# Kernel tuning notes

Hardware: AMD Instinct MI355X
Metric: run time of the kernel (lower is better)

The kernel has to match this reference:

```python
import jax, jax.numpy as jnp
import numpy as np

EPS = 1e-12  # torch F.normalize eps


def _l2norm(x, axis):
    return x / jnp.maximum(jnp.linalg.norm(x, axis=axis, keepdims=True), EPS)


def setup_inputs() -> dict:
    key = jax.random.key(0)
    ks = jax.random.split(key, 8)
    B, N, D_in, H, K, D_out = 16, 1024, 1024, 512, 64, 1024
    return {
        "input_data": jax.random.normal(ks[0], (B, N, D_in), dtype=jnp.float32),
        "fc1_w": jax.random.normal(ks[1], (H, D_in), dtype=jnp.float32) * 0.02,
        "fc1_b": jax.random.normal(ks[2], (H,), dtype=jnp.float32) * 0.02,
        "conv_w": jax.random.normal(ks[3], (K, H), dtype=jnp.float32) * 0.1,
        "conv_b": jax.random.normal(ks[4], (K,), dtype=jnp.float32) * 0.1,
        "centroids": jax.random.normal(ks[5], (K, H), dtype=jnp.float32),
        "fc2_w": jax.random.normal(ks[6], (D_out, K * H), dtype=jnp.float32) * 0.01,
        "fc2_b": jax.random.normal(ks[7], (D_out,), dtype=jnp.float32) * 0.01,
    }


def reference(input_data, fc1_w, fc1_b, conv_w, conv_b, centroids, fc2_w, fc2_b):
    # fc1 + relu: [B, N, H]
    h = jax.nn.relu(jnp.einsum('bnd,hd->bnh', input_data, fc1_w) + fc1_b)
    # NetVLAD input layout: [B, H, N] (the (N,1) spatial dims collapse to N)
    x = jnp.swapaxes(h, 1, 2)
    # normalize descriptors across feature dim (F.normalize(x, p=2, dim=1))
    xn = _l2norm(x, axis=1)
    # 1x1-conv soft assignment -> softmax over clusters: [B, K, N]
    logits = jnp.einsum('kh,bhn->bkn', conv_w, xn) + conv_b[None, :, None]
    a = jax.nn.softmax(logits, axis=1)
    # vlad_{bkh} = sum_n a_{bkn} (xn_{bhn} - c_{kh})  (fused, no [B,K,H,N] tensor)
    vlad = jnp.einsum('bkn,bhn->bkh', a, xn) - a.sum(axis=-1)[:, :, None] * centroids[None]
    vlad = _l2norm(vlad, axis=2)              # intra-normalization
    vlad = vlad.reshape(vlad.shape[0], -1)    # [B, K*H]
    vlad = _l2norm(vlad, axis=1)              # global L2 norm
    # fc2 + relu: [B, out_dim]
    return jax.nn.relu(vlad @ fc2_w.T + fc2_b)
```

## Files before the change

kernel.cpp:

```cpp
#include <hip/hip_runtime.h>
#include <hip/hip_bf16.h>

typedef __bf16  bf16x8 __attribute__((ext_vector_type(8)));
typedef float   f32x4  __attribute__((ext_vector_type(4)));

#define DEV __device__ __forceinline__

DEV ushort f2b(float f){
  union { float f; unsigned u; } c; c.f = f;
  unsigned u = c.u;
  unsigned r = (u + 0x7FFFu + ((u >> 16) & 1u)) >> 16;
  return (ushort)r;
}
DEV float b2f(ushort h){
  union { unsigned u; float f; } c; c.u = ((unsigned)h) << 16;
  return c.f;
}
DEV float wredsum(float v){
  #pragma unroll
  for(int o = 32; o > 0; o >>= 1) v += __shfl_xor(v, o, 64);
  return v;
}
DEV float wredmax(float v){
  #pragma unroll
  for(int o = 32; o > 0; o >>= 1) v = fmaxf(v, __shfl_xor(v, o, 64));
  return v;
}
DEV void gload_lds16(const void* g, void* l){
  __builtin_amdgcn_global_load_lds(
      (const __attribute__((address_space(1))) void*)g,
      (__attribute__((address_space(3))) void*)l,
      16, 0, 0);
}
DEV bf16x8 cvt8(float4 a0, float4 a1){
  bf16x8 t;
  t[0]=(__bf16)a0.x; t[1]=(__bf16)a0.y; t[2]=(__bf16)a0.z; t[3]=(__bf16)a0.w;
  t[4]=(__bf16)a1.x; t[5]=(__bf16)a1.y; t[6]=(__bf16)a1.z; t[7]=(__bf16)a1.w;
  return t;
}

__global__ void prep(const float* __restrict__ W1, const float* __restrict__ CW,
                     const float* __restrict__ CB,
                     ushort* __restrict__ W1b, ushort* __restrict__ CWb,
                     float* __restrict__ CBp){
  int bid = blockIdx.x, tid = threadIdx.x;
  if(bid < 512){
    int i = bid * 256 + tid;
    float4 f = ((const float4*)W1)[i];
    ushort4 o; o.x = f2b(f.x); o.y = f2b(f.y); o.z = f2b(f.z); o.w = f2b(f.w);
    ((ushort4*)W1b)[i] = o;
  } else if(bid < 640){
    int i = (bid - 512) * 256 + tid;
    int k = i >> 9, h = i & 511;
    int seg = h >> 3, pos = h & 7;
    CWb[(k << 9) + ((seg ^ (k & 7)) << 3) + pos] = f2b(CW[i]);
  } else {
    if(tid < 128) CBp[tid] = (tid < 64) ? CB[tid] : 0.0f;
  }
}

__global__ __launch_bounds__(512) void fc1sm(
    const float* __restrict__ A, const ushort* __restrict__ B,
    const float* __restrict__ bias, const ushort* __restrict__ CWb,
    const float* __restrict__ CBp, ushort* __restrict__ XNT,
    ushort* __restrict__ AThi, ushort* __restrict__ ATlo)
{
  const int K = 1024;
  __shared__ __align__(16) char smem[149504];
  __shared__ float ssq_p[4][64];
  __shared__ float scale_s[64];
  const int tid = threadIdx.x, lane = tid & 63, wid = tid >> 6;
  const int bm0 = blockIdx.x * 64;
  const int wr = (wid >> 2) * 32;
  const int wc = (wid & 3) * 128;
  const int wcol = wid & 3;

  const int srow = tid >> 3;
  const int sseg = tid & 7;
  const char* asrc = (const char*)A + (size_t)(bm0 + srow) * 4096
                     + (sseg ^ (srow & 7)) * 16;
  const int bslot = (tid & 3) ^ ((tid >> 3) & 3);
  const ushort* bg = B + (size_t)(tid >> 2) * K + bslot * 8;

  f32x4 acc[2][8];
  #pragma unroll
  for(int i = 0; i < 2; i++)
    #pragma unroll
    for(int j = 0; j < 8; j++) acc[i][j] = (f32x4){0.f, 0.f, 0.f, 0.f};

  const int arow = lane & 15;
  const int khalf = lane >> 4;

#define STAGE_F1N(buf, kb) do { \
    gload_lds16(asrc + (kb), smem + (buf) * 8192 + tid * 16); \
    const ushort* bs_ = bg + ((kb) >> 2); \
    char* bd_ = smem + 16384 + (buf) * 32768 + tid * 16; \
    gload_lds16(bs_,           bd_); \
    gload_lds16(bs_ + 128 * K, bd_ + 8192); \
    gload_lds16(bs_ + 256 * K, bd_ + 16384); \
    gload_lds16(bs_ + 384 * K, bd_ + 24576); \
  } while(0)

  STAGE_F1N(0, 0);
  __syncthreads();

  int cur = 0;
  for(int ks = 0; ks < 32; ++ks){
    if(ks + 1 < 32) STAGE_F1N(cur ^ 1, (ks + 1) * 128);
    bf16x8 af[2], bfr[8];
    #pragma unroll
    for(int mi = 0; mi < 2; mi++){
      int r = wr + mi * 16 + arow;
      const char* base = smem + cur * 8192 + r * 128;
      float4 a0 = *(const float4*)(base + (((khalf * 2)     ^ (r & 7)) * 16));
      float4 a1 = *(const float4*)(base + (((khalf * 2 + 1) ^ (r & 7)) * 16));
      af[mi] = cvt8(a0, a1);
    }
    #pragma unroll
    for(int ni = 0; ni < 8; ni++){
      int r = wc + ni * 16 + arow;
      bfr[ni] = *(const bf16x8*)(smem + 16384 + cur * 32768
                                 + r * 64 + ((khalf ^ ((r >> 1) & 3)) * 16));
    }
    #pragma unroll
    for(int mi = 0; mi < 2; mi++)
      #pragma unroll
      for(int ni = 0; ni < 8; ni++)
        acc[mi][ni] = __builtin_amdgcn_mfma_f32_16x16x32_bf16(af[mi], bfr[ni], acc[mi][ni], 0, 0, 0);
    __syncthreads();
    cur ^= 1;
  }
#undef STAGE_F1N

  float bv[8];
  #pragma unroll
  for(int ni = 0; ni < 8; ni++) bv[ni] = bias[wc + ni * 16 + (lane & 15)];
  float p[2][4];
  #pragma unroll
  for(int mi = 0; mi < 2; mi++)
    #pragma unroll
    for(int i = 0; i < 4; i++){
      float s = 0.f;
      #pragma unroll
      for(int ni = 0; ni < 8; ni++){
        float v = fmaxf(acc[mi][ni][i] + bv[ni], 0.f);
        acc[mi][ni][i] = v;
        s += v * v;
      }
      p[mi][i] = s;
    }
  #pragma unroll
  for(int o = 1; o < 16; o <<= 1)
    #pragma unroll
    for(int mi = 0; mi < 2; mi++)
      #pragma unroll
      for(int i = 0; i < 4; i++)
        p[mi][i] += __shfl_xor(p[mi][i], o, 64);
  if((lane & 15) == 0){
    int g = lane >> 4;
    #pragma unroll
    for(int mi = 0; mi < 2; mi++)
      #pragma unroll
      for(int i = 0; i < 4; i++)
        ssq_p[wcol][wr + mi * 16 + g * 4 + i] = p[mi][i];
  }
  __syncthreads();
  if(tid < 64){
    float s = ssq_p[0][tid] + ssq_p[1][tid] + ssq_p[2][tid] + ssq_p[3][tid];
    scale_s[tid] = 1.0f / fmaxf(sqrtf(s), 1e-12f);
  }
  __syncthreads();

  ushort* Tb  = (ushort*)(smem + 81920);
  ushort* xnm = (ushort*)smem;
  #pragma unroll
  for(int mi = 0; mi < 2; mi++)
    #pragma unroll
    for(int i = 0; i < 4; i++){
      int rt = wr + mi * 16 + (lane >> 4) * 4 + i;
      float sc = scale_s[rt];
      #pragma unroll
      for(int ni = 0; ni < 8; ni++){
        int h = wc + ni * 16 + (lane & 15);
        ushort v = f2b(acc[mi][ni][i] * sc);
        Tb[h * 66 + rt] = v;
        xnm[rt * 520 + h] = v;
      }
    }
  __syncthreads();

  const int bb = bm0 >> 10, n0b = bm0 & 1023;
  {
    const char* tb = (const char*)smem + 81920 + tid * 132;
    unsigned tmp[32];
    #pragma unroll
    for(int j = 0; j < 32; j++) tmp[j] = *(const unsigned*)(tb + j * 4);
    ushort* dst = XNT + ((size_t)bb * 512 + tid) * 1024 + n0b;
    #pragma unroll
    for(int u = 0; u < 8; u++){
      uint4 w; w.x = tmp[u*4]; w.y = tmp[u*4+1]; w.z = tmp[u*4+2]; w.w = tmp[u*4+3];
      *(uint4*)(dst + u * 8) = w;
    }
  }
  __syncthreads();

  char* CWs = smem + 66560;
  #pragma unroll
  for(int pp = 0; pp < 8; pp++)
    gload_lds16((const char*)CWb + pp * 8192 + tid * 16, CWs + pp * 8192 + tid * 16);
  __syncthreads();

  float* as_ = (float*)(smem + 132096);
  const int nt = (wid >> 2) * 32, kt = (wid & 3) * 16;
  f32x4 acc2[2];
  acc2[0] = (f32x4){0.f,0.f,0.f,0.f};
  acc2[1] = (f32x4){0.f,0.f,0.f,0.f};
  const int kr = kt + arow;
  #pragma unroll
  for(int s = 0; s < 16; ++s){
    bf16x8 a0 = *(const bf16x8*)(smem + (size_t)(nt + arow) * 1040 + s * 64 + khalf * 16);
    bf16x8 a1 = *(const bf16x8*)(smem + (size_t)(nt + 16 + arow) * 1040 + s * 64 + khalf * 16);
    bf16x8 bw = *(const bf16x8*)(CWs + kr * 1024 + (((s * 4 + khalf) ^ (kr & 7)) * 16));
    acc2[0] = __builtin_amdgcn_mfma_f32_16x16x32_bf16(a0, bw, acc2[0], 0, 0, 0);
    acc2[1] = __builtin_amdgcn_mfma_f32_16x16x32_bf16(a1, bw, acc2[1], 0, 0, 0);
  }
  {
    float bv2 = CBp[kt + (lane & 15)];
    #pragma unroll
    for(int mi = 0; mi < 2; mi++)
      #pragma unroll
      for(int i = 0; i < 4; i++)
        as_[(nt + mi * 16 + (lane >> 4) * 4 + i) * 65 + kt + (lane & 15)] = acc2[mi][i] + bv2;
  }
  __syncthreads();

  #pragma unroll
  for(int i = 0; i < 8; i++){
    int rl = wid * 8 + i;
    float l = as_[rl * 65 + lane];
    float m = wredmax(l);
    float e = __expf(l - m);
    float s = wredsum(e);
    as_[rl * 65 + lane] = e / s;
  }
  __syncthreads();

  {
    const int nl = tid & 63, kq = tid >> 6;
    #pragma unroll
    for(int q = 0; q < 8; q++){
      int k = kq * 8 + q;
      float a = as_[nl * 65 + k];
      ushort hi = f2b(a);
      float lo = a - b2f(hi);
      size_t idx = ((size_t)bb * 64 + k) * 1024 + n0b + nl;
      AThi[idx] = hi;
      ATlo[idx] = f2b(lo);
    }
  }
}

__global__ __launch_bounds__(512) void vlad_mfma(
    const ushort* __restrict__ AThi, const ushort* __restrict__ ATlo,
    const ushort* __restrict__ XNT, const float* __restrict__ cent,
    ushort* __restrict__ vlb, float* __restrict__ ssq)
{
  __shared__ __align__(16) ushort Ah[2][16 * 32];
  __shared__ __align__(16) ushort Al[2][16 * 32];
  __shared__ __align__(16) ushort Xs[2][512 * 32];
  __shared__ float red[8][16];
  __shared__ float scale_s[16], ssqn_s[16];
  const int tid = threadIdx.x, lane = tid & 63, wid = tid >> 6;
  const int b = blockIdx.x, kg = blockIdx.y;
  const int k0 = kg * 16;
  const int hw = wid;
  const int arow = lane & 15, khalf = lane >> 4;

  const int xslot = (tid & 3) ^ ((tid >> 3) & 3);
  const ushort* xg = XNT + ((size_t)b * 512 + (tid >> 2)) * 1024 + xslot * 8;
  const int aslot = (lane & 3) ^ ((lane >> 3) & 3);
  const ushort* ahg = AThi + ((size_t)b * 64 + k0 + (lane >> 2)) * 1024 + aslot * 8;
  const ushort* alg = ATlo + ((size_t)b * 64 + k0 + (lane >> 2)) * 1024 + aslot * 8;

  f32x4 acc[4];
  #pragma unroll
  for(int i = 0; i < 4; i++) acc[i] = (f32x4){0.f, 0.f, 0.f, 0.f};
  f32x4 asum = (f32x4){0.f, 0.f, 0.f, 0.f};
  bf16x8 ones;
  #pragma unroll
  for(int j = 0; j < 8; j++) ones[j] = (__bf16)1.0f;

#define STAGE_VL(buf, n0v) do { \
    char* xd = (char*)&Xs[buf][0] + tid * 16; \
    gload_lds16(xg + (n0v),                xd); \
    gload_lds16(xg + (n0v) + 128 * 1024,   xd + 8192); \
    gload_lds16(xg + (n0v) + 256 * 1024,   xd + 16384); \
    gload_lds16(xg + (n0v) + 384 * 1024,   xd + 24576); \
    if(wid == 0)      gload_lds16(ahg + (n0v), (char*)&Ah[buf][0] + lane * 16); \
    else if(wid == 1) gload_lds16(alg + (n0v), (char*)&Al[buf][0] + lane * 16); \
  } while(0)

  STAGE_VL(0, 0);
  __syncthreads();

  int cur = 0;
  for(int ks = 0; ks < 32; ++ks){
    if(ks + 1 < 32) STAGE_VL(cur ^ 1, (ks + 1) * 32);
    bf16x8 ah, al, bfr[4];
    {
      int sl = khalf ^ ((arow >> 1) & 3);
      ah = *(const bf16x8*)&Ah[cur][arow * 32 + sl * 8];
      al = *(const bf16x8*)&Al[cur][arow * 32 + sl * 8];
    }
    #pragma unroll
    for(int ni = 0; ni < 4; ni++){
      int r = hw * 64 + ni * 16 + arow;
      bfr[ni] = *(const bf16x8*)&Xs[cur][r * 32 + ((khalf ^ ((r >> 1) & 3)) * 8)];
    }
    asum = __builtin_amdgcn_mfma_f32_16x16x32_bf16(ah, ones, asum, 0, 0, 0);
    asum = __builtin_amdgcn_mfma_f32_16x16x32_bf16(al, ones, asum, 0, 0, 0);
    #pragma unroll
    for(int ni = 0; ni < 4; ni++){
      acc[ni] = __builtin_amdgcn_mfma_f32_16x16x32_bf16(ah, bfr[ni], acc[ni], 0, 0, 0);
      acc[ni] = __builtin_amdgcn_mfma_f32_16x16x32_bf16(al, bfr[ni], acc[ni], 0, 0, 0);
    }
    __syncthreads();
    cur ^= 1;
  }
#undef STAGE_VL

  float vl[4][4];
  #pragma unroll
  for(int ni = 0; ni < 4; ni++)
    #pragma unroll
    for(int i = 0; i < 4; i++){
      int r_ = (lane >> 4) * 4 + i;
      int h = hw * 64 + ni * 16 + (lane & 15);
      vl[ni][i] = acc[ni][i] - asum[i] * cent[(size_t)(k0 + r_) * 512 + h];
    }
  float sq[4];
  #pragma unroll
  for(int i = 0; i < 4; i++){
    float s = 0.f;
    #pragma unroll
    for(int ni = 0; ni < 4; ni++) s += vl[ni][i] * vl[ni][i];
    sq[i] = s;
  }
  #pragma unroll
  for(int o = 1; o < 16; o <<= 1)
    #pragma unroll
    for(int i = 0; i < 4; i++) sq[i] += __shfl_xor(sq[i], o, 64);
  if((lane & 15) == 0){
    #pragma unroll
    for(int i = 0; i < 4; i++) red[hw][(lane >> 4) * 4 + i] = sq[i];
  }
  __syncthreads();
  if(tid < 16){
    float s = 0.f;
    #pragma unroll
    for(int w = 0; w < 8; w++) s += red[w][tid];
    float sc = 1.0f / fmaxf(sqrtf(s), 1e-12f);
    scale_s[tid] = sc;
    ssqn_s[tid] = s * sc * sc;
  }
  __syncthreads();
  if(tid < 4)
    ssq[b * 16 + kg * 4 + tid] = ssqn_s[tid * 4] + ssqn_s[tid * 4 + 1]
                               + ssqn_s[tid * 4 + 2] + ssqn_s[tid * 4 + 3];
  #pragma unroll
  for(int ni = 0; ni < 4; ni++)
    #pragma unroll
    for(int i = 0; i < 4; i++){
      int r_ = (lane >> 4) * 4 + i;
      int h = hw * 64 + ni * 16 + (lane & 15);
      vlb[(size_t)b * 32768 + (size_t)(k0 + r_) * 512 + h] = f2b(vl[ni][i] * scale_s[r_]);
    }
}

__global__ __launch_bounds__(256) void fc2_mfma(const float* __restrict__ W,
                                                const ushort* __restrict__ vlb,
                                                float* __restrict__ part){
  __shared__ __align__(16) float Bs[2][128 * 32];
  const int tid = threadIdx.x, lane = tid & 63, wid = tid >> 6;
  const int c0 = blockIdx.x * 128;
  const int kc = blockIdx.y;
  const size_t kbase = (size_t)kc * 256;

  const int srow = tid >> 3;
  const int seg  = tid & 7;
  f32x4 acc0 = (f32x4){0.f,0.f,0.f,0.f};
  f32x4 acc1 = (f32x4){0.f,0.f,0.f,0.f};

  const int arow = lane & 15;
  const int khalf = lane >> 4;
  const int cRow0 = wid * 32 + (lane & 15);
  const int cRow1 = cRow0 + 16;

  #pragma unroll
  for(int pass = 0; pass < 4; ++pass){
    int row = pass * 32 + srow;
    const char* src = (const char*)W + (size_t)(c0 + row) * 131072
                      + kbase * 4 + ((seg ^ (row & 7)) * 16);
    gload_lds16(src, (char*)&Bs[0][0] + row * 128 + seg * 16);
  }
  __syncthreads();

  int cur = 0;
  for(int ks = 0; ks < 8; ++ks){
    if(ks + 1 < 8){
      #pragma unroll
      for(int pass = 0; pass < 4; ++pass){
        int row = pass * 32 + srow;
        const char* src = (const char*)W + (size_t)(c0 + row) * 131072
                          + (kbase + (ks + 1) * 32) * 4 + ((seg ^ (row & 7)) * 16);
        gload_lds16(src, (char*)&Bs[cur ^ 1][0] + row * 128 + seg * 16);
      }
    }
    bf16x8 af = *(const bf16x8*)((const char*)vlb + (size_t)arow * 65536
                                 + (kbase + ks * 32 + khalf * 8) * 2);
    int t0 = khalf * 2;
    const char* bsc = (const char*)&Bs[cur][0];
    float4 b00 = *(const float4*)(bsc + cRow0 * 128 + ((t0     ^ (cRow0 & 7)) * 16));
    float4 b01 = *(const float4*)(bsc + cRow0 * 128 + (((t0+1) ^ (cRow0 & 7)) * 16));
    float4 b10 = *(const float4*)(bsc + cRow1 * 128 + ((t0     ^ (cRow1 & 7)) * 16));
    float4 b11 = *(const float4*)(bsc + cRow1 * 128 + (((t0+1) ^ (cRow1 & 7)) * 16));
    bf16x8 bf0 = cvt8(b00, b01);
    bf16x8 bf1 = cvt8(b10, b11);

    acc0 = __builtin_amdgcn_mfma_f32_16x16x32_bf16(af, bf0, acc0, 0, 0, 0);
    acc1 = __builtin_amdgcn_mfma_f32_16x16x32_bf16(af, bf1, acc1, 0, 0, 0);
    __syncthreads();
    cur ^= 1;
  }

  #pragma unroll
  for(int i = 0; i < 4; ++i){
    int b = (lane >> 4) * 4 + i;
    int d0 = c0 + wid * 32 + (lane & 15);
    part[((size_t)kc * 16 + b) * 1024 + d0]      = acc0[i];
    part[((size_t)kc * 16 + b) * 1024 + d0 + 16] = acc1[i];
  }
}

__global__ __launch_bounds__(256) void fin(const float* __restrict__ part, const float* __restrict__ ssq,
                                           const float* __restrict__ b2, float* __restrict__ out){
  __shared__ float red[4][64];
  int lane = threadIdx.x & 63, wq = threadIdx.x >> 6;
  int o = blockIdx.x * 64 + lane;
  int b = o >> 10, d = o & 1023;
  float s = 0;
  #pragma unroll
  for(int i = 0; i < 32; i++){
    int t = wq * 32 + i;
    s += part[((size_t)t * 16 + b) * 1024 + d];
  }
  red[wq][lane] = s;
  __syncthreads();
  if(wq == 0){
    float g = 0;
    #pragma unroll
    for(int kg = 0; kg < 16; kg++) g += ssq[b * 16 + kg];
    float gsv = 1.0f / fmaxf(sqrtf(g), 1e-12f);
    float tot = red[0][lane] + red[1][lane] + red[2][lane] + red[3][lane];
    out[o] = fmaxf(gsv * tot + b2[d], 0.0f);
  }
}

extern "C" void kernel_launch(void* const* d_in, const int* in_sizes, int n_in,
                              void* d_out, int out_size, void* d_ws, size_t ws_size,
                              hipStream_t stream){
  const float* X    = (const float*)d_in[0];
  const float* W1   = (const float*)d_in[1];
  const float* B1   = (const float*)d_in[2];
  const float* CW   = (const float*)d_in[3];
  const float* CB   = (const float*)d_in[4];
  const float* CENT = (const float*)d_in[5];
  const float* W2   = (const float*)d_in[6];
  const float* B2   = (const float*)d_in[7];
  float* out = (float*)d_out;
  char* ws = (char*)d_ws;

  ushort* W1b  = (ushort*)(ws + 0);
  ushort* CWb  = (ushort*)(ws + 1048576);
  float*  CBp  = (float*) (ws + 1114112);
  ushort* XNT  = (ushort*)(ws + 1114624);
  ushort* AThi = (ushort*)(ws + 17891840);
  ushort* ATlo = (ushort*)(ws + 19988992);
  ushort* VLb  = (ushort*)(ws + 22086144);
  float*  SSQ  = (float*) (ws + 23134720);
  float*  PART = (float*) (ws + 23135744);

  prep<<<641, 256, 0, stream>>>(W1, CW, CB, W1b, CWb, CBp);
  fc1sm<<<256, 512, 0, stream>>>(X, W1b, B1, CWb, CBp, XNT, AThi, ATlo);
  vlad_mfma<<<dim3(16, 4), 512, 0, stream>>>(AThi, ATlo, XNT, CENT, VLb, SSQ);
  fc2_mfma<<<dim3(8, 128), 256, 0, stream>>>(W2, VLb, PART);
  fin<<<256, 256, 0, stream>>>(PART, SSQ, B2, out);
}
```

Baseline: 110.5 us.

## Drop LDS staging in fc1 GEMM and split softmax/transposed-store across warps

```diff
diff --git a/kernel.cpp b/kernel.cpp
--- a/kernel.cpp
+++ b/kernel.cpp
@@ -15,16 +15,6 @@
 DEV float b2f(ushort h){
   union { unsigned u; float f; } c; c.u = ((unsigned)h) << 16;
   return c.f;
-}
-DEV float wredsum(float v){
-  #pragma unroll
-  for(int o = 32; o > 0; o >>= 1) v += __shfl_xor(v, o, 64);
-  return v;
-}
-DEV float wredmax(float v){
-  #pragma unroll
-  for(int o = 32; o > 0; o >>= 1) v = fmaxf(v, __shfl_xor(v, o, 64));
-  return v;
 }
 DEV void gload_lds16(const void* g, void* l){
   __builtin_amdgcn_global_load_lds(
@@ -51,9 +41,7 @@
     ((ushort4*)W1b)[i] = o;
   } else if(bid < 640){
     int i = (bid - 512) * 256 + tid;
-    int k = i >> 9, h = i & 511;
-    int seg = h >> 3, pos = h & 7;
-    CWb[(k << 9) + ((seg ^ (k & 7)) << 3) + pos] = f2b(CW[i]);
+    CWb[i] = f2b(CW[i]);
   } else {
     if(tid < 128) CBp[tid] = (tid < 64) ? CB[tid] : 0.0f;
   }
@@ -65,8 +53,7 @@
     const float* __restrict__ CBp, ushort* __restrict__ XNT,
     ushort* __restrict__ AThi, ushort* __restrict__ ATlo)
 {
-  const int K = 1024;
-  __shared__ __align__(16) char smem[149504];
+  __shared__ __align__(16) ushort xnm[64 * 520];
   __shared__ float ssq_p[4][64];
   __shared__ float scale_s[64];
   const int tid = threadIdx.x, lane = tid & 63, wid = tid >> 6;
@@ -74,13 +61,15 @@
   const int wr = (wid >> 2) * 32;
   const int wc = (wid & 3) * 128;
   const int wcol = wid & 3;
-
-  const int srow = tid >> 3;
-  const int sseg = tid & 7;
-  const char* asrc = (const char*)A + (size_t)(bm0 + srow) * 4096
-                     + (sseg ^ (srow & 7)) * 16;
-  const int bslot = (tid & 3) ^ ((tid >> 3) & 3);
-  const ushort* bg = B + (size_t)(tid >> 2) * K + bslot * 8;
+  const int arow = lane & 15;
+  const int g16  = lane >> 4;
+
+  const float*  a0p = A + (size_t)(bm0 + wr + arow) * 1024;
+  const float*  a1p = a0p + (size_t)16 * 1024;
+  const ushort* bp[8];
+  #pragma unroll
+  for(int ni = 0; ni < 8; ni++)
+    bp[ni] = B + (size_t)(wc + ni * 16 + arow) * 1024;
 
   f32x4 acc[2][8];
   #pragma unroll
@@ -88,53 +77,31 @@
     #pragma unroll
     for(int j = 0; j < 8; j++) acc[i][j] = (f32x4){0.f, 0.f, 0.f, 0.f};
 
-  const int arow = lane & 15;
-  const int khalf = lane >> 4;
-
-#define STAGE_F1N(buf, kb) do { \
-    gload_lds16(asrc + (kb), smem + (buf) * 8192 + tid * 16); \
-    const ushort* bs_ = bg + ((kb) >> 2); \
-    char* bd_ = smem + 16384 + (buf) * 32768 + tid * 16; \
-    gload_lds16(bs_,           bd_); \
-    gload_lds16(bs_ + 128 * K, bd_ + 8192); \
-    gload_lds16(bs_ + 256 * K, bd_ + 16384); \
-    gload_lds16(bs_ + 384 * K, bd_ + 24576); \
-  } while(0)
-
-  STAGE_F1N(0, 0);
-  __syncthreads();
-
-  int cur = 0;
+  #pragma unroll 4
   for(int ks = 0; ks < 32; ++ks){
-    if(ks + 1 < 32) STAGE_F1N(cur ^ 1, (ks + 1) * 128);
+    const int ko = ks * 32 + g16 * 8;
     bf16x8 af[2], bfr[8];
-    #pragma unroll
-    for(int mi = 0; mi < 2; mi++){
-      int r = wr + mi * 16 + arow;
-      const char* base = smem + cur * 8192 + r * 128;
-      float4 a0 = *(const float4*)(base + (((khalf * 2)     ^ (r & 7)) * 16));
-      float4 a1 = *(const float4*)(base + (((khalf * 2 + 1) ^ (r & 7)) * 16));
-      af[mi] = cvt8(a0, a1);
-    }
-    #pragma unroll
-    for(int ni = 0; ni < 8; ni++){
-      int r = wc + ni * 16 + arow;
-      bfr[ni] = *(const bf16x8*)(smem + 16384 + cur * 32768
-                                 + r * 64 + ((khalf ^ ((r >> 1) & 3)) * 16));
-    }
+    {
+      float4 x0 = *(const float4*)(a0p + ko);
+      float4 x1 = *(const float4*)(a0p + ko + 4);
+      af[0] = cvt8(x0, x1);
+      float4 y0 = *(const float4*)(a1p + ko);
+      float4 y1 = *(const float4*)(a1p + ko + 4);
+      af[1] = cvt8(y0, y1);
+    }
+    #pragma unroll
+    for(int ni = 0; ni < 8; ni++)
+      bfr[ni] = *(const bf16x8*)(bp[ni] + ko);
     #pragma unroll
     for(int mi = 0; mi < 2; mi++)
       #pragma unroll
       for(int ni = 0; ni < 8; ni++)
         acc[mi][ni] = __builtin_amdgcn_mfma_f32_16x16x32_bf16(af[mi], bfr[ni], acc[mi][ni], 0, 0, 0);
-    __syncthreads();
-    cur ^= 1;
-  }
-#undef STAGE_F1N
+  }
 
   float bv[8];
   #pragma unroll
-  for(int ni = 0; ni < 8; ni++) bv[ni] = bias[wc + ni * 16 + (lane & 15)];
+  for(int ni = 0; ni < 8; ni++) bv[ni] = bias[wc + ni * 16 + arow];
   float p[2][4];
   #pragma unroll
   for(int mi = 0; mi < 2; mi++)
@@ -156,13 +123,12 @@
       #pragma unroll
       for(int i = 0; i < 4; i++)
         p[mi][i] += __shfl_xor(p[mi][i], o, 64);
-  if((lane & 15) == 0){
-    int g = lane >> 4;
+  if(arow == 0){
     #pragma unroll
     for(int mi = 0; mi < 2; mi++)
       #pragma unroll
       for(int i = 0; i < 4; i++)
-        ssq_p[wcol][wr + mi * 16 + g * 4 + i] = p[mi][i];
+        ssq_p[wcol][wr + mi * 16 + g16 * 4 + i] = p[mi][i];
   }
   __syncthreads();
   if(tid < 64){
@@ -171,91 +137,89 @@
   }
   __syncthreads();
 
-  ushort* Tb  = (ushort*)(smem + 81920);
-  ushort* xnm = (ushort*)smem;
   #pragma unroll
   for(int mi = 0; mi < 2; mi++)
     #pragma unroll
     for(int i = 0; i < 4; i++){
-      int rt = wr + mi * 16 + (lane >> 4) * 4 + i;
+      int rt = wr + mi * 16 + g16 * 4 + i;
       float sc = scale_s[rt];
       #pragma unroll
       for(int ni = 0; ni < 8; ni++){
-        int h = wc + ni * 16 + (lane & 15);
-        ushort v = f2b(acc[mi][ni][i] * sc);
-        Tb[h * 66 + rt] = v;
-        xnm[rt * 520 + h] = v;
+        int h = wc + ni * 16 + arow;
+        xnm[rt * 520 + h] = f2b(acc[mi][ni][i] * sc);
       }
     }
   __syncthreads();
 
   const int bb = bm0 >> 10, n0b = bm0 & 1023;
-  {
-    const char* tb = (const char*)smem + 81920 + tid * 132;
-    unsigned tmp[32];
-    #pragma unroll
-    for(int j = 0; j < 32; j++) tmp[j] = *(const unsigned*)(tb + j * 4);
-    ushort* dst = XNT + ((size_t)bb * 512 + tid) * 1024 + n0b;
-    #pragma unroll
-    for(int u = 0; u < 8; u++){
-      uint4 w; w.x = tmp[u*4]; w.y = tmp[u*4+1]; w.z = tmp[u*4+2]; w.w = tmp[u*4+3];
-      *(uint4*)(dst + u * 8) = w;
-    }
-  }
-  __syncthreads();
-
-  char* CWs = smem + 66560;
-  #pragma unroll
-  for(int pp = 0; pp < 8; pp++)
-    gload_lds16((const char*)CWb + pp * 8192 + tid * 16, CWs + pp * 8192 + tid * 16);
-  __syncthreads();
-
-  float* as_ = (float*)(smem + 132096);
-  const int nt = (wid >> 2) * 32, kt = (wid & 3) * 16;
-  f32x4 acc2[2];
-  acc2[0] = (f32x4){0.f,0.f,0.f,0.f};
-  acc2[1] = (f32x4){0.f,0.f,0.f,0.f};
-  const int kr = kt + arow;
-  #pragma unroll
-  for(int s = 0; s < 16; ++s){
-    bf16x8 a0 = *(const bf16x8*)(smem + (size_t)(nt + arow) * 1040 + s * 64 + khalf * 16);
-    bf16x8 a1 = *(const bf16x8*)(smem + (size_t)(nt + 16 + arow) * 1040 + s * 64 + khalf * 16);
-    bf16x8 bw = *(const bf16x8*)(CWs + kr * 1024 + (((s * 4 + khalf) ^ (kr & 7)) * 16));
-    acc2[0] = __builtin_amdgcn_mfma_f32_16x16x32_bf16(a0, bw, acc2[0], 0, 0, 0);
-    acc2[1] = __builtin_amdgcn_mfma_f32_16x16x32_bf16(a1, bw, acc2[1], 0, 0, 0);
-  }
-  {
-    float bv2 = CBp[kt + (lane & 15)];
-    #pragma unroll
-    for(int mi = 0; mi < 2; mi++)
-      #pragma unroll
-      for(int i = 0; i < 4; i++)
-        as_[(nt + mi * 16 + (lane >> 4) * 4 + i) * 65 + kt + (lane & 15)] = acc2[mi][i] + bv2;
-  }
-  __syncthreads();
-
-  #pragma unroll
-  for(int i = 0; i < 8; i++){
-    int rl = wid * 8 + i;
-    float l = as_[rl * 65 + lane];
-    float m = wredmax(l);
-    float e = __expf(l - m);
-    float s = wredsum(e);
-    as_[rl * 65 + lane] = e / s;
-  }
-  __syncthreads();
-
-  {
-    const int nl = tid & 63, kq = tid >> 6;
-    #pragma unroll
-    for(int q = 0; q < 8; q++){
-      int k = kq * 8 + q;
-      float a = as_[nl * 65 + k];
-      ushort hi = f2b(a);
-      float lo = a - b2f(hi);
-      size_t idx = ((size_t)bb * 64 + k) * 1024 + n0b + nl;
-      AThi[idx] = hi;
-      ATlo[idx] = f2b(lo);
+
+  if(wid < 4){
+    const int t = wid, c = arow;
+    f32x4 lg[4];
+    #pragma unroll
+    for(int kf = 0; kf < 4; kf++) lg[kf] = (f32x4){0.f,0.f,0.f,0.f};
+    const ushort* cw0 = CWb + (size_t)c * 512 + g16 * 8;
+    const char*   xb0 = (const char*)xnm + (t * 16 + c) * 1040 + g16 * 16;
+    #pragma unroll
+    for(int s = 0; s < 16; ++s){
+      bf16x8 xb = *(const bf16x8*)(xb0 + s * 64);
+      #pragma unroll
+      for(int kf = 0; kf < 4; kf++){
+        bf16x8 cwf = *(const bf16x8*)(cw0 + (size_t)kf * 16 * 512 + s * 32);
+        lg[kf] = __builtin_amdgcn_mfma_f32_16x16x32_bf16(cwf, xb, lg[kf], 0, 0, 0);
+      }
+    }
+    float l[4][4];
+    float m = -3.4e38f;
+    #pragma unroll
+    for(int kf = 0; kf < 4; kf++)
+      #pragma unroll
+      for(int i = 0; i < 4; i++){
+        l[kf][i] = lg[kf][i] + CBp[kf * 16 + g16 * 4 + i];
+        m = fmaxf(m, l[kf][i]);
+      }
+    m = fmaxf(m, __shfl_xor(m, 16, 64));
+    m = fmaxf(m, __shfl_xor(m, 32, 64));
+    float s = 0.f;
+    #pragma unroll
+    for(int kf = 0; kf < 4; kf++)
+      #pragma unroll
+      for(int i = 0; i < 4; i++){
+        l[kf][i] = __expf(l[kf][i] - m);
+        s += l[kf][i];
+      }
+    s += __shfl_xor(s, 16, 64);
+    s += __shfl_xor(s, 32, 64);
+    float inv = 1.0f / s;
+    #pragma unroll
+    for(int kf = 0; kf < 4; kf++)
+      #pragma unroll
+      for(int i = 0; i < 4; i++){
+        float a = l[kf][i] * inv;
+        ushort hi = f2b(a);
+        float lo = a - b2f(hi);
+        int k = kf * 16 + g16 * 4 + i;
+        size_t idx = ((size_t)bb * 64 + k) * 1024 + n0b + t * 16 + c;
+        AThi[idx] = hi;
+        ATlo[idx] = f2b(lo);
+      }
+  } else {
+    #pragma unroll
+    for(int rep = 0; rep < 2; rep++){
+      int h = (tid - 256) + rep * 256;
+      unsigned tmp[32];
+      #pragma unroll
+      for(int j = 0; j < 32; j++){
+        unsigned lo = xnm[(2 * j)     * 520 + h];
+        unsigned hi = xnm[(2 * j + 1) * 520 + h];
+        tmp[j] = lo | (hi << 16);
+      }
+      ushort* dst = XNT + ((size_t)bb * 512 + h) * 1024 + n0b;
+      #pragma unroll
+      for(int u = 0; u < 8; u++){
+        uint4 w; w.x = tmp[u*4]; w.y = tmp[u*4+1]; w.z = tmp[u*4+2]; w.w = tmp[u*4+3];
+        *(uint4*)(dst + u * 8) = w;
+      }
     }
   }
 }
```

Result: slower. 161.9 us (+46.6%).
